# Kernel tuning notes

Hardware: AMD Instinct MI355X
Metric: run time of the kernel (lower is better)

## Reference

```python
import jax, jax.numpy as jnp
import numpy as np
import math

B, S = 4, 1024
V, D, L, H, F, MAXLEN = 32000, 1024, 6, 16, 4096, 2048
DH = D // H
NUM_BUCKETS, MAX_DIST = 32, 256
REL_SCALE = 64.0 ** 0.5
EPS = 1e-5


def setup_inputs() -> dict:
    key = jax.random.key(0)
    ks = iter(jax.random.split(key, 32))
    sd = 0.02
    inp = {
        'src': jax.random.randint(next(ks), (B, S), 0, V),
        'src_mask': jnp.ones((B, 1, 1, S), dtype=jnp.int32),
        'tok_emb': jax.random.normal(next(ks), (V, D), jnp.float32) * sd,
        'pos_emb': jax.random.normal(next(ks), (MAXLEN, D), jnp.float32) * sd,
        'Wq': jax.random.normal(next(ks), (L, D, D), jnp.float32) * sd,
        'bq': jnp.zeros((L, D), jnp.float32),
        'Wk': jax.random.normal(next(ks), (L, D, D), jnp.float32) * sd,
        'bk': jnp.zeros((L, D), jnp.float32),
        'Wv': jax.random.normal(next(ks), (L, D, D), jnp.float32) * sd,
        'bv': jnp.zeros((L, D), jnp.float32),
        'Wo': jax.random.normal(next(ks), (L, D, D), jnp.float32) * sd,
        'bo': jnp.zeros((L, D), jnp.float32),
        'rel_bias': jax.random.normal(next(ks), (L, NUM_BUCKETS, H), jnp.float32) * sd,
        'ln1_g': jnp.ones((L, D), jnp.float32),
        'ln1_b': jnp.zeros((L, D), jnp.float32),
        'W1': jax.random.normal(next(ks), (L, D, F), jnp.float32) * sd,
        'b1': jnp.zeros((L, F), jnp.float32),
        'W2': jax.random.normal(next(ks), (L, F, D), jnp.float32) * sd,
        'b2': jnp.zeros((L, D), jnp.float32),
        'ln2_g': jnp.ones((L, D), jnp.float32),
        'ln2_b': jnp.zeros((L, D), jnp.float32),
    }
    return inp


def _rel_pos_bucket(seq_len):
    # non-causal bucketing (T5-style), matching the torch source
    q = jnp.arange(seq_len)
    k = jnp.arange(seq_len)
    n = q[:, None] - k[None, :]          # == -(k - q)
    nb = NUM_BUCKETS // 2                # 16
    ret = (n < 0).astype(jnp.int32) * nb
    n = jnp.abs(n)
    max_exact = nb // 2                  # 8
    is_small = n < max_exact
    val_large = max_exact + (
        jnp.log(jnp.maximum(n, 1).astype(jnp.float32) / max_exact)
        / math.log(MAX_DIST / max_exact) * (nb - max_exact)
    ).astype(jnp.int32)
    val_large = jnp.minimum(val_large, nb - 1)
    return ret + jnp.where(is_small, n, val_large)  # [S,S] in [0,32)


def _layer_norm(x, g, b):
    mu = jnp.mean(x, axis=-1, keepdims=True)
    var = jnp.var(x, axis=-1, keepdims=True)
    return (x - mu) * jax.lax.rsqrt(var + EPS) * g + b


def reference(src, src_mask, tok_emb, pos_emb, Wq, bq, Wk, bk, Wv, bv, Wo, bo,
              rel_bias, ln1_g, ln1_b, W1, b1, W2, b2, ln2_g, ln2_b):
    seq_len = src.shape[1]
    bucket = _rel_pos_bucket(seq_len)                      # [S,S] int
    x = tok_emb[src] * jnp.sqrt(jnp.float32(D)) + pos_emb[jnp.arange(seq_len)][None]
    scale = jnp.sqrt(jnp.float32(DH))
    neg = jnp.float32(-1e10)

    def layer(x, p):
        (wq, bq_, wk, bk_, wv, bv_, wo, bo_, rb, g1, b1_, w1, bb1, w2, bb2, g2, b2_) = p
        Q = (x @ wq + bq_).reshape(B, seq_len, H, DH)
        K = (x @ wk + bk_).reshape(B, seq_len, H, DH)
        Vv = (x @ wv + bv_).reshape(B, seq_len, H, DH)
        energy = jnp.einsum('bqhd,bkhd->bhqk', Q, K) / scale
        energy = jnp.where(src_mask == 0, neg, energy)
        bias = rb[bucket]                                  # [S,S,H]
        energy = energy + jnp.transpose(bias, (2, 0, 1))[None] * REL_SCALE
        attn = jax.nn.softmax(energy, axis=-1)
        o = jnp.einsum('bhqk,bkhd->bqhd', attn, Vv).reshape(B, seq_len, D)
        o = o @ wo + bo_
        x = _layer_norm(x + o, g1, b1_)
        f = jax.nn.relu(x @ w1 + bb1) @ w2 + bb2
        x = _layer_norm(x + f, g2, b2_)
        return x, None

    params = (Wq, bq, Wk, bk, Wv, bv, Wo, bo, rel_bias,
              ln1_g, ln1_b, W1, b1, W2, b2, ln2_g, ln2_b)
    x, _ = jax.lax.scan(layer, x, params)
    return x
```

## Files before the change

### kernel.cpp

```cpp
#include <hip/hip_runtime.h>

#define B_ 4
#define S_ 1024
#define D_ 1024
#define F_ 4096
#define H_ 16
#define L_ 6
#define M_ (B_*S_)

typedef unsigned short u16;
typedef __attribute__((ext_vector_type(4))) unsigned short u16x4;
typedef __attribute__((ext_vector_type(8))) short s16x8;
typedef __attribute__((ext_vector_type(8))) __bf16 bf16x8;
typedef __attribute__((ext_vector_type(4))) float f32x4;

typedef const __attribute__((address_space(1))) unsigned int gu32;
typedef __attribute__((address_space(3))) unsigned int su32;

__device__ __forceinline__ u16 f2bf(float f) {
  union { float f; unsigned u; } v; v.f = f;
  unsigned u = v.u;
  return (u16)((u + 0x7fffu + ((u >> 16) & 1u)) >> 16);
}

__device__ __forceinline__ f32x4 mfma16(s16x8 a, s16x8 b, f32x4 c) {
  return __builtin_amdgcn_mfma_f32_16x16x32_bf16(
      __builtin_bit_cast(bf16x8, a), __builtin_bit_cast(bf16x8, b), c, 0, 0, 0);
}

__device__ __forceinline__ void gload16(const void* g, void* s) {
  __builtin_amdgcn_global_load_lds((gu32*)g, (su32*)s, 16, 0, 0);
}

__device__ __forceinline__ s16x8 lds_swz(const u16* base, int row, int cb) {
  const int addr = row * 128 + (cb ^ ((row & 7) << 4));
  return *(const s16x8*)((const char*)base + addr);
}

__global__ __launch_bounds__(256) void transpose_cvt(
    const float* __restrict__ src, u16* __restrict__ dst, int R, int Cc)
{
  __shared__ float t[32][33];
  const int c0 = blockIdx.x * 32, r0 = blockIdx.y * 32;
  const int tx = threadIdx.x & 31, ty = threadIdx.x >> 5;
#pragma unroll
  for (int i = 0; i < 4; i++)
    t[ty + 8 * i][tx] = src[(size_t)(r0 + ty + 8 * i) * Cc + c0 + tx];
  __syncthreads();
#pragma unroll
  for (int i = 0; i < 4; i++)
    dst[(size_t)(c0 + ty + 8 * i) * R + r0 + tx] = f2bf(t[tx][ty + 8 * i]);
}

__global__ __launch_bounds__(256) void transpose4(
    const float* __restrict__ Wq, const float* __restrict__ Wk,
    const float* __restrict__ Wv, const float* __restrict__ Wo,
    u16* __restrict__ WTqkv, u16* __restrict__ WTo)
{
  __shared__ float t[32][33];
  const int z = blockIdx.z;
  const float* src = (z == 0) ? Wq : (z == 1) ? Wk : (z == 2) ? Wv : Wo;
  u16* dst = (z < 3) ? WTqkv + (size_t)z * D_ * D_ : WTo;
  const int c0 = blockIdx.x * 32, r0 = blockIdx.y * 32;
  const int tx = threadIdx.x & 31, ty = threadIdx.x >> 5;
#pragma unroll
  for (int i = 0; i < 4; i++)
    t[ty + 8 * i][tx] = src[(size_t)(r0 + ty + 8 * i) * D_ + c0 + tx];
  __syncthreads();
#pragma unroll
  for (int i = 0; i < 4; i++)
    dst[(size_t)(c0 + ty + 8 * i) * D_ + r0 + tx] = f2bf(t[tx][ty + 8 * i]);
}

template<int OUTMODE>
__device__ __forceinline__ void gemm128_body(
    const u16* __restrict__ A, const u16* __restrict__ Bt,
    const float* __restrict__ bias, float* __restrict__ Cf,
    u16* __restrict__ Ch, int N, int K, int kbeg, int kend, float scale)
{
  __shared__ __align__(16) u16 As[128 * 64];
  __shared__ __align__(16) u16 Bs[128 * 64];
  const int tid = threadIdx.x, lane = tid & 63, w = tid >> 6;
  const int bm = blockIdx.x * 128, bn = blockIdx.y * 128;
  const int wm = (w >> 1) * 64, wn = (w & 1) * 64;

  f32x4 acc[4][4];
#pragma unroll
  for (int i = 0; i < 4; i++)
#pragma unroll
    for (int j = 0; j < 4; j++) acc[i][j] = {0.f, 0.f, 0.f, 0.f};

  for (int k0 = kbeg; k0 < kend; k0 += 64) {
    __syncthreads();
#pragma unroll
    for (int i = 0; i < 4; i++) {
      const int flat = i * 4096 + w * 1024 + lane * 16;
      const int row = flat >> 7, ce = (flat & 127) >> 1;
      gload16(A + (size_t)(bm + row) * K + k0 + ce, As + i * 2048 + w * 512);
      gload16(Bt + (size_t)(bn + row) * K + k0 + ce, Bs + i * 2048 + w * 512);
    }
    __syncthreads();
#pragma unroll
    for (int kk = 0; kk < 2; kk++) {
      s16x8 af[4], bf[4];
#pragma unroll
      for (int mf = 0; mf < 4; mf++)
        af[mf] = *(const s16x8*)&As[(wm + mf * 16 + (lane & 15)) * 64 + kk * 32 + (lane >> 4) * 8];
#pragma unroll
      for (int nf = 0; nf < 4; nf++)
        bf[nf] = *(const s16x8*)&Bs[(wn + nf * 16 + (lane & 15)) * 64 + kk * 32 + (lane >> 4) * 8];
#pragma unroll
      for (int mf = 0; mf < 4; mf++)
#pragma unroll
        for (int nf = 0; nf < 4; nf++)
          acc[mf][nf] = mfma16(af[mf], bf[nf], acc[mf][nf]);
    }
  }
#pragma unroll
  for (int nf = 0; nf < 4; nf++) {
    const int col = bn + wn + nf * 16 + (lane & 15);
    const float bv = (OUTMODE == 0) ? 0.f : bias[col];
#pragma unroll
    for (int mf = 0; mf < 4; mf++) {
#pragma unroll
      for (int j = 0; j < 4; j++) {
        const int row = bm + wm + mf * 16 + ((lane >> 4) << 2) + j;
        float v = acc[mf][nf][j];
        if (OUTMODE == 0) {
          Cf[(size_t)row * N + col] = v;
        } else {
          v = (v + bv) * scale;
          if (OUTMODE == 2) v = fmaxf(v, 0.f);
          Ch[(size_t)row * N + col] = f2bf(v);
        }
      }
    }
  }
}

__global__ __launch_bounds__(256, 3) void gemm_qkv(
    const u16* __restrict__ A, const u16* __restrict__ WT,
    const float* __restrict__ bq, const float* __restrict__ bk,
    const float* __restrict__ bv, u16* __restrict__ Out)
{
  const int z = blockIdx.z;
  const float* bias = (z == 0) ? bq : (z == 1) ? bk : bv;
  gemm128_body<1>(A, WT + (size_t)z * D_ * D_, bias, nullptr,
                  Out + (size_t)z * M_ * D_, D_, D_, 0, D_,
                  (z == 0) ? 0.125f : 1.0f);
}

__global__ __launch_bounds__(256, 3) void gemm_ffn1(
    const u16* __restrict__ A, const u16* __restrict__ WT,
    const float* __restrict__ bias, u16* __restrict__ Out)
{
  gemm128_body<2>(A, WT, bias, nullptr, Out, F_, D_, 0, D_, 1.0f);
}

__global__ __launch_bounds__(256, 3) void gemm_splitk(
    const u16* __restrict__ A, const u16* __restrict__ WT,
    float* __restrict__ P, int N, int K)
{
  const int z = blockIdx.z;
  const int half = K >> 1;
  gemm128_body<0>(A, WT, nullptr, P + (size_t)z * M_ * (size_t)N, nullptr,
                  N, K, z * half, z * half + half, 1.0f);
}

__global__ __launch_bounds__(256) void vt_transpose(
    const u16* __restrict__ Vb, u16* __restrict__ Vt)
{
  __shared__ u16 t[64][66];
  const int s0 = blockIdx.x * 64;
  const int bh = blockIdx.y;
  const int b = bh >> 4, h = bh & 15;
  const int tid = threadIdx.x;
  const int row = tid >> 2;
  const int c0 = (tid & 3) * 16;
  const u16* src = Vb + (size_t)(b * S_ + s0 + row) * D_ + h * 64 + c0;
  *(s16x8*)&t[row][c0] = *(const s16x8*)src;
  *(s16x8*)&t[row][c0 + 8] = *(const s16x8*)(src + 8);
  __syncthreads();
  const int dh = tid >> 2;
  const int sc = (tid & 3) * 16;
  s16x8 a, bv;
#pragma unroll
  for (int u = 0; u < 8; u++) a[u] = (short)t[sc + u][dh];
#pragma unroll
  for (int u = 0; u < 8; u++) bv[u] = (short)t[sc + 8 + u][dh];
  u16* dst = Vt + (size_t)(bh * 64 + dh) * S_ + s0 + sc;
  *(s16x8*)dst = a;
  *(s16x8*)(dst + 8) = bv;
}

__global__ __launch_bounds__(256, 4) void attn_kernel(
    const u16* __restrict__ Qb, const u16* __restrict__ Kb,
    const u16* __restrict__ Vt, const int* __restrict__ mask,
    const float* __restrict__ rb, u16* __restrict__ AO)
{
  __shared__ float lut[2048];
  __shared__ __align__(16) u16 Ks[64 * 64];
  __shared__ __align__(16) u16 Vs[64 * 64];
  __shared__ __align__(16) u16 Ps[4][16 * 68];

  const int tid = threadIdx.x;
  const int lane = tid & 63;
  const int w = tid >> 6;
  const int bh = blockIdx.x;
  const int b = bh >> 4, h = bh & 15;
  const int q0 = blockIdx.y * 64 + w * 16;
  const int bS = b * S_, hh = h * 64;

  for (int idx = tid; idx < 2048; idx += 256) {
    const int rel = idx - 1024;
    const int ret = rel < 0 ? 16 : 0;
    const int n = rel < 0 ? -rel : rel;
    int bu;
    if (n < 8) bu = ret + n;
    else {
      const float t = logf((float)n * 0.125f) * (8.0f / 3.4657359027997265f);
      int vl = 8 + (int)t;
      if (vl > 15) vl = 15;
      bu = ret + vl;
    }
    lut[idx] = rb[bu * 16 + h] * 8.0f;
  }

  s16x8 qf[2];
#pragma unroll
  for (int kk = 0; kk < 2; kk++)
    qf[kk] = *(const s16x8*)(Qb + (size_t)(bS + q0 + (lane & 15)) * D_ + hh +
                             kk * 32 + (lane >> 4) * 8);

  f32x4 oacc[4];
#pragma unroll
  for (int i = 0; i < 4; i++) oacc[i] = {0.f, 0.f, 0.f, 0.f};
  float rm[4], rl[4];
#pragma unroll
  for (int j = 0; j < 4; j++) { rm[j] = -3e38f; rl[j] = 0.f; }

  for (int kt = 0; kt < S_; kt += 64) {
    __syncthreads();
#pragma unroll
    for (int i = 0; i < 2; i++) {
      const int flat = i * 4096 + w * 1024 + lane * 16;
      const int row = flat >> 7;
      const int ce = ((flat & 127) ^ ((row & 7) << 4)) >> 1;
      gload16(Kb + (size_t)(bS + kt + row) * D_ + hh + ce, Ks + i * 2048 + w * 512);
      gload16(Vt + (size_t)(bh * 64 + row) * S_ + kt + ce, Vs + i * 2048 + w * 512);
    }
    __syncthreads();

    f32x4 sacc[4];
#pragma unroll
    for (int i = 0; i < 4; i++) sacc[i] = {0.f, 0.f, 0.f, 0.f};
#pragma unroll
    for (int kk = 0; kk < 2; kk++) {
      const int cb = kk * 64 + (lane >> 4) * 16;
#pragma unroll
      for (int nf = 0; nf < 4; nf++) {
        const s16x8 kb = lds_swz(Ks, nf * 16 + (lane & 15), cb);
        sacc[nf] = mfma16(qf[kk], kb, sacc[nf]);
      }
    }

    int km[4];
#pragma unroll
    for (int nf = 0; nf < 4; nf++)
      km[nf] = mask[bS + kt + nf * 16 + (lane & 15)];

    const int lidx0 = q0 + (lane >> 4) * 4 + 1024 - kt - (lane & 15);
#pragma unroll
    for (int j = 0; j < 4; j++) {
      const int lrow = ((lane >> 4) << 2) + j;
      float sc[4];
      float mx = -3e38f;
#pragma unroll
      for (int nf = 0; nf < 4; nf++) {
        float s = (km[nf] == 0) ? -1e10f : sacc[nf][j];
        s += lut[lidx0 + j - nf * 16];
        sc[nf] = s;
        mx = fmaxf(mx, s);
      }
      mx = fmaxf(mx, __shfl_xor(mx, 1));
      mx = fmaxf(mx, __shfl_xor(mx, 2));
      mx = fmaxf(mx, __shfl_xor(mx, 4));
      mx = fmaxf(mx, __shfl_xor(mx, 8));
      const float m_new = fmaxf(rm[j], mx);
      const float fs = __expf(rm[j] - m_new);
      rm[j] = m_new;
      float psum = 0.f;
#pragma unroll
      for (int nf = 0; nf < 4; nf++) {
        const float p = __expf(sc[nf] - m_new);
        psum += p;
        Ps[w][lrow * 68 + nf * 16 + (lane & 15)] = f2bf(p);
      }
      psum += __shfl_xor(psum, 1);
      psum += __shfl_xor(psum, 2);
      psum += __shfl_xor(psum, 4);
      psum += __shfl_xor(psum, 8);
      rl[j] = rl[j] * fs + psum;
#pragma unroll
      for (int df = 0; df < 4; df++) oacc[df][j] *= fs;
    }

#pragma unroll
    for (int kk = 0; kk < 2; kk++) {
      const s16x8 pa = *(const s16x8*)&Ps[w][(lane & 15) * 68 + kk * 32 + (lane >> 4) * 8];
      const int cb = kk * 64 + (lane >> 4) * 16;
#pragma unroll
      for (int df = 0; df < 4; df++) {
        const s16x8 vb = lds_swz(Vs, df * 16 + (lane & 15), cb);
        oacc[df] = mfma16(pa, vb, oacc[df]);
      }
    }
  }

  float inv[4];
#pragma unroll
  for (int j = 0; j < 4; j++) inv[j] = 1.0f / rl[j];
#pragma unroll
  for (int df = 0; df < 4; df++)
#pragma unroll
    for (int j = 0; j < 4; j++) {
      const int qrow = q0 + ((lane >> 4) << 2) + j;
      AO[(size_t)(bS + qrow) * D_ + hh + df * 16 + (lane & 15)] =
          f2bf(oacc[df][j] * inv[j]);
    }
}

__global__ __launch_bounds__(256) void ln_fused(
    const float* __restrict__ X, const float* __restrict__ P0,
    const float* __restrict__ P1, const float* __restrict__ bias,
    const float* __restrict__ g, const float* __restrict__ be,
    float* __restrict__ Yf, u16* __restrict__ Yh)
{
  const int row = blockIdx.x;
  const int tid = threadIdx.x;
  const float4 xv = ((const float4*)(X + (size_t)row * D_))[tid];
  const float4 p0 = ((const float4*)(P0 + (size_t)row * D_))[tid];
  const float4 p1 = ((const float4*)(P1 + (size_t)row * D_))[tid];
  const float4 bb = ((const float4*)bias)[tid];
  const float v0 = xv.x + p0.x + p1.x + bb.x;
  const float v1 = xv.y + p0.y + p1.y + bb.y;
  const float v2 = xv.z + p0.z + p1.z + bb.z;
  const float v3 = xv.w + p0.w + p1.w + bb.w;
  float sum = v0 + v1 + v2 + v3;
  float ss = v0 * v0 + v1 * v1 + v2 * v2 + v3 * v3;
#pragma unroll
  for (int o = 1; o < 64; o <<= 1) {
    sum += __shfl_xor(sum, o);
    ss += __shfl_xor(ss, o);
  }
  __shared__ float s1[4], s2[4];
  if ((tid & 63) == 0) { s1[tid >> 6] = sum; s2[tid >> 6] = ss; }
  __syncthreads();
  sum = s1[0] + s1[1] + s1[2] + s1[3];
  ss = s2[0] + s2[1] + s2[2] + s2[3];
  const float mu = sum * (1.f / D_);
  const float var = ss * (1.f / D_) - mu * mu;
  const float rstd = rsqrtf(var + 1e-5f);
  const float4 gv = ((const float4*)g)[tid];
  const float4 bv = ((const float4*)be)[tid];
  float4 y;
  y.x = (v0 - mu) * rstd * gv.x + bv.x;
  y.y = (v1 - mu) * rstd * gv.y + bv.y;
  y.z = (v2 - mu) * rstd * gv.z + bv.z;
  y.w = (v3 - mu) * rstd * gv.w + bv.w;
  ((float4*)(Yf + (size_t)row * D_))[tid] = y;
  u16x4 hv;
  hv.x = f2bf(y.x); hv.y = f2bf(y.y); hv.z = f2bf(y.z); hv.w = f2bf(y.w);
  ((u16x4*)(Yh + (size_t)row * D_))[tid] = hv;
}

__global__ __launch_bounds__(256) void embed_kernel(
    const int* __restrict__ src, const float* __restrict__ tok,
    const float* __restrict__ pos, float* __restrict__ X, u16* __restrict__ Xh)
{
  const int row = blockIdx.x;
  const int s = row & (S_ - 1);
  const int t = src[row];
  const int tid = threadIdx.x;
  const float4 tv = ((const float4*)(tok + (size_t)t * D_))[tid];
  const float4 pv = ((const float4*)(pos + (size_t)s * D_))[tid];
  float4 y;
  y.x = tv.x * 32.f + pv.x;
  y.y = tv.y * 32.f + pv.y;
  y.z = tv.z * 32.f + pv.z;
  y.w = tv.w * 32.f + pv.w;
  ((float4*)(X + (size_t)row * D_))[tid] = y;
  u16x4 hv;
  hv.x = f2bf(y.x); hv.y = f2bf(y.y); hv.z = f2bf(y.z); hv.w = f2bf(y.w);
  ((u16x4*)(Xh + (size_t)row * D_))[tid] = hv;
}

extern "C" void kernel_launch(void* const* d_in, const int* in_sizes, int n_in,
                              void* d_out, int out_size, void* d_ws, size_t ws_size,
                              hipStream_t stream)
{
  const int* src = (const int*)d_in[0];
  const int* mask = (const int*)d_in[1];
  const float* tok_emb = (const float*)d_in[2];
  const float* pos_emb = (const float*)d_in[3];
  const float* Wq = (const float*)d_in[4];
  const float* bq = (const float*)d_in[5];
  const float* Wk = (const float*)d_in[6];
  const float* bk = (const float*)d_in[7];
  const float* Wv = (const float*)d_in[8];
  const float* bv = (const float*)d_in[9];
  const float* Wo = (const float*)d_in[10];
  const float* bo = (const float*)d_in[11];
  const float* rb = (const float*)d_in[12];
  const float* g1 = (const float*)d_in[13];
  const float* b1n = (const float*)d_in[14];
  const float* W1 = (const float*)d_in[15];
  const float* b1f = (const float*)d_in[16];
  const float* W2 = (const float*)d_in[17];
  const float* b2f = (const float*)d_in[18];
  const float* g2 = (const float*)d_in[19];
  const float* b2n = (const float*)d_in[20];
  float* out = (float*)d_out;

  char* ws = (char*)d_ws;
  const size_t MB = 1ull << 20;
  float* xb   = (float*)(ws + 0);
  u16*   xb16 = (u16*)(ws + 16 * MB);
  u16*   Qb16 = (u16*)(ws + 24 * MB);
  u16*   Kb16 = (u16*)(ws + 32 * MB);
  u16*   Vb16 = (u16*)(ws + 40 * MB);
  u16*   Vt16 = (u16*)(ws + 48 * MB);
  u16*   AO16 = (u16*)(ws + 40 * MB);
  float* OPp  = (float*)(ws + 48 * MB);
  u16*   Hb16 = (u16*)(ws + 24 * MB);
  float* Fp   = (float*)(ws + 56 * MB);
  u16* WTqkv  = (u16*)(ws + 88 * MB);
  u16* WTo    = (u16*)(ws + 94 * MB);
  u16* WT1    = (u16*)(ws + 96 * MB);
  u16* WT2    = (u16*)(ws + 104 * MB);

  embed_kernel<<<M_, 256, 0, stream>>>(src, tok_emb, pos_emb, xb, xb16);

  for (int l = 0; l < L_; l++) {
    const size_t oDD = (size_t)l * D_ * D_;
    const size_t oDF = (size_t)l * D_ * F_;

    transpose4<<<dim3(32, 32, 4), 256, 0, stream>>>(
        Wq + oDD, Wk + oDD, Wv + oDD, Wo + oDD, WTqkv, WTo);
    transpose_cvt<<<dim3(F_ / 32, D_ / 32), 256, 0, stream>>>(W1 + oDF, WT1, D_, F_);
    transpose_cvt<<<dim3(D_ / 32, F_ / 32), 256, 0, stream>>>(W2 + oDF, WT2, F_, D_);

    gemm_qkv<<<dim3(M_ / 128, D_ / 128, 3), 256, 0, stream>>>(
        xb16, WTqkv, bq + l * D_, bk + l * D_, bv + l * D_, Qb16);

    vt_transpose<<<dim3(S_ / 64, B_ * H_), 256, 0, stream>>>(Vb16, Vt16);

    attn_kernel<<<dim3(B_ * H_, S_ / 64), 256, 0, stream>>>(
        Qb16, Kb16, Vt16, mask, rb + l * 32 * H_, AO16);

    gemm_splitk<<<dim3(M_ / 128, D_ / 128, 2), 256, 0, stream>>>(
        AO16, WTo, OPp, D_, D_);

    ln_fused<<<M_, 256, 0, stream>>>(
        xb, OPp, OPp + (size_t)M_ * D_, bo + l * D_,
        g1 + l * D_, b1n + l * D_, xb, xb16);

    gemm_ffn1<<<dim3(M_ / 128, F_ / 128), 256, 0, stream>>>(
        xb16, WT1, b1f + l * F_, Hb16);

    gemm_splitk<<<dim3(M_ / 128, D_ / 128, 2), 256, 0, stream>>>(
        Hb16, WT2, Fp, D_, F_);

    ln_fused<<<M_, 256, 0, stream>>>(
        xb, Fp, Fp + (size_t)M_ * D_, b2f + l * D_,
        g2 + l * D_, b2n + l * D_, (l == L_ - 1) ? out : xb, xb16);
  }
}
```

Before: 1.511 ms.

## Replace 128x128 GEMM with double-buffered 256x256 pipelined MFMA kernel and split-K 4

```diff
diff --git a/kernel.cpp b/kernel.cpp
--- a/kernel.cpp
+++ b/kernel.cpp
@@ -32,99 +32,133 @@
   __builtin_amdgcn_global_load_lds((gu32*)g, (su32*)s, 16, 0, 0);
 }
 
-__device__ __forceinline__ s16x8 lds_swz(const u16* base, int row, int cb) {
-  const int addr = row * 128 + (cb ^ ((row & 7) << 4));
-  return *(const s16x8*)((const char*)base + addr);
-}
-
-__global__ __launch_bounds__(256) void transpose_cvt(
-    const float* __restrict__ src, u16* __restrict__ dst, int R, int Cc)
-{
-  __shared__ float t[32][33];
-  const int c0 = blockIdx.x * 32, r0 = blockIdx.y * 32;
-  const int tx = threadIdx.x & 31, ty = threadIdx.x >> 5;
-#pragma unroll
-  for (int i = 0; i < 4; i++)
-    t[ty + 8 * i][tx] = src[(size_t)(r0 + ty + 8 * i) * Cc + c0 + tx];
-  __syncthreads();
-#pragma unroll
-  for (int i = 0; i < 4; i++)
-    dst[(size_t)(c0 + ty + 8 * i) * R + r0 + tx] = f2bf(t[tx][ty + 8 * i]);
-}
-
-__global__ __launch_bounds__(256) void transpose4(
-    const float* __restrict__ Wq, const float* __restrict__ Wk,
-    const float* __restrict__ Wv, const float* __restrict__ Wo,
-    u16* __restrict__ WTqkv, u16* __restrict__ WTo)
-{
-  __shared__ float t[32][33];
-  const int z = blockIdx.z;
-  const float* src = (z == 0) ? Wq : (z == 1) ? Wk : (z == 2) ? Wv : Wo;
-  u16* dst = (z < 3) ? WTqkv + (size_t)z * D_ * D_ : WTo;
-  const int c0 = blockIdx.x * 32, r0 = blockIdx.y * 32;
-  const int tx = threadIdx.x & 31, ty = threadIdx.x >> 5;
-#pragma unroll
-  for (int i = 0; i < 4; i++)
-    t[ty + 8 * i][tx] = src[(size_t)(r0 + ty + 8 * i) * D_ + c0 + tx];
-  __syncthreads();
-#pragma unroll
-  for (int i = 0; i < 4; i++)
-    dst[(size_t)(c0 + ty + 8 * i) * D_ + r0 + tx] = f2bf(t[tx][ty + 8 * i]);
-}
+__device__ __forceinline__ s16x8 readfrag(const u16* half, int r, int kk, int hi4) {
+  const int c = (kk * 64 + hi4 * 16) ^ ((r & 7) << 4);
+  return *(const s16x8*)((const char*)half + r * 128 + c);
+}
+
+__device__ __forceinline__ void stage_half(
+    const u16* __restrict__ src, int ldk, u16* lds_half, int w, int lane)
+{
+#pragma unroll
+  for (int j = 0; j < 2; j++) {
+    const int flat = j * 8192 + w * 1024 + lane * 16;
+    const int row = flat >> 7;
+    const int kb = (flat & 127) ^ ((row & 7) << 4);
+    gload16(src + (size_t)row * ldk + (kb >> 1), lds_half + j * 4096 + w * 512);
+  }
+}
+
+#define BAR     asm volatile("s_barrier" ::: "memory")
+#define PH_PRE  asm volatile("s_barrier" ::: "memory"); __builtin_amdgcn_s_setprio(1)
+#define PH_POST __builtin_amdgcn_s_setprio(0); __builtin_amdgcn_sched_barrier(0)
+#define VM4     asm volatile("s_waitcnt vmcnt(4)" ::: "memory")
+#define VM0     asm volatile("s_waitcnt vmcnt(0)" ::: "memory")
+
+#define READ_B(bufhalf) do { \
+  _Pragma("unroll") for (int nf = 0; nf < 4; nf++) \
+  _Pragma("unroll") for (int kk = 0; kk < 2; kk++) \
+    bfr[nf][kk] = readfrag(bufhalf, rb0 + nf * 16 + lo16, kk, hi4); } while (0)
+#define READ_A(bufhalf, Q) do { \
+  _Pragma("unroll") for (int m = 0; m < 2; m++) \
+  _Pragma("unroll") for (int kk = 0; kk < 2; kk++) \
+    af[m][kk] = readfrag(bufhalf, (2 * (Q) + m) * 16 + lo16, kk, hi4); } while (0)
+#define DO_MFMA(Q) do { \
+  _Pragma("unroll") for (int kk = 0; kk < 2; kk++) \
+  _Pragma("unroll") for (int m = 0; m < 2; m++) \
+  _Pragma("unroll") for (int nf = 0; nf < 4; nf++) \
+    acc[2 * (Q) + m][nf] = mfma16(af[m][kk], bfr[nf][kk], acc[2 * (Q) + m][nf]); } while (0)
 
 template<int OUTMODE>
-__device__ __forceinline__ void gemm128_body(
+__device__ __forceinline__ void gemm256_body(
     const u16* __restrict__ A, const u16* __restrict__ Bt,
     const float* __restrict__ bias, float* __restrict__ Cf,
-    u16* __restrict__ Ch, int N, int K, int kbeg, int kend, float scale)
-{
-  __shared__ __align__(16) u16 As[128 * 64];
-  __shared__ __align__(16) u16 Bs[128 * 64];
+    u16* __restrict__ Ch, int N, int K, int kbeg, int kslice, float scale)
+{
+  __shared__ __align__(16) u16 As[2][2][8192];
+  __shared__ __align__(16) u16 Bs[2][2][8192];
   const int tid = threadIdx.x, lane = tid & 63, w = tid >> 6;
-  const int bm = blockIdx.x * 128, bn = blockIdx.y * 128;
-  const int wm = (w >> 1) * 64, wn = (w & 1) * 64;
-
-  f32x4 acc[4][4];
-#pragma unroll
-  for (int i = 0; i < 4; i++)
+  const int wr = w >> 2, wc = w & 3;
+  const int lo16 = lane & 15, hi4 = lane >> 4;
+  const int bm = blockIdx.x * 256, bn = blockIdx.y * 256;
+  const int rb0 = (wc & 1) * 64;
+
+  const u16* Abase = A + (size_t)bm * K + kbeg;
+  const u16* Bbase = Bt + (size_t)bn * K + kbeg;
+  const size_t h1 = (size_t)128 * K;
+  const int NT = kslice >> 6, NI = NT >> 1;
+
+  f32x4 acc[8][4];
+#pragma unroll
+  for (int i = 0; i < 8; i++)
 #pragma unroll
     for (int j = 0; j < 4; j++) acc[i][j] = {0.f, 0.f, 0.f, 0.f};
 
-  for (int k0 = kbeg; k0 < kend; k0 += 64) {
-    __syncthreads();
-#pragma unroll
-    for (int i = 0; i < 4; i++) {
-      const int flat = i * 4096 + w * 1024 + lane * 16;
-      const int row = flat >> 7, ce = (flat & 127) >> 1;
-      gload16(A + (size_t)(bm + row) * K + k0 + ce, As + i * 2048 + w * 512);
-      gload16(Bt + (size_t)(bn + row) * K + k0 + ce, Bs + i * 2048 + w * 512);
-    }
-    __syncthreads();
-#pragma unroll
-    for (int kk = 0; kk < 2; kk++) {
-      s16x8 af[4], bf[4];
-#pragma unroll
-      for (int mf = 0; mf < 4; mf++)
-        af[mf] = *(const s16x8*)&As[(wm + mf * 16 + (lane & 15)) * 64 + kk * 32 + (lane >> 4) * 8];
-#pragma unroll
-      for (int nf = 0; nf < 4; nf++)
-        bf[nf] = *(const s16x8*)&Bs[(wn + nf * 16 + (lane & 15)) * 64 + kk * 32 + (lane >> 4) * 8];
-#pragma unroll
-      for (int mf = 0; mf < 4; mf++)
-#pragma unroll
-        for (int nf = 0; nf < 4; nf++)
-          acc[mf][nf] = mfma16(af[mf], bf[nf], acc[mf][nf]);
-    }
-  }
+  stage_half(Abase,           K, As[0][0], w, lane);
+  stage_half(Abase + h1,      K, As[0][1], w, lane);
+  stage_half(Bbase,           K, Bs[0][0], w, lane);
+  stage_half(Bbase + h1,      K, Bs[0][1], w, lane);
+  stage_half(Abase + 64,      K, As[1][0], w, lane);
+  stage_half(Abase + h1 + 64, K, As[1][1], w, lane);
+  stage_half(Bbase + 64,      K, Bs[1][0], w, lane);
+  stage_half(Bbase + h1 + 64, K, Bs[1][1], w, lane);
+  asm volatile("s_waitcnt vmcnt(8)" ::: "memory");
+  BAR;
+
+  const u16* Ae = As[0][wr]; const u16* Ao = As[1][wr];
+  const u16* Be = Bs[0][wc >> 1]; const u16* Bo = Bs[1][wc >> 1];
+  s16x8 af[2][2], bfr[4][2];
+
+  for (int it = 0; it < NI - 1; ++it) {
+    READ_B(Be); READ_A(Ae, 0);
+    if (it > 0) {
+      stage_half(Abase +      (size_t)(2 * it + 1) * 64, K, As[1][0], w, lane);
+      stage_half(Abase + h1 + (size_t)(2 * it + 1) * 64, K, As[1][1], w, lane);
+    }
+    PH_PRE; DO_MFMA(0); PH_POST; BAR;
+    READ_A(Ae, 1);
+    stage_half(Bbase +      (size_t)(2 * it + 2) * 64, K, Bs[0][0], w, lane);
+    PH_PRE; DO_MFMA(1); PH_POST; BAR;
+    READ_A(Ae, 2);
+    stage_half(Bbase + h1 + (size_t)(2 * it + 2) * 64, K, Bs[0][1], w, lane);
+    PH_PRE; DO_MFMA(2); PH_POST; BAR;
+    READ_A(Ae, 3);
+    PH_PRE; DO_MFMA(3); PH_POST; VM4; BAR;
+    READ_B(Bo); READ_A(Ao, 0);
+    stage_half(Abase +      (size_t)(2 * it + 2) * 64, K, As[0][0], w, lane);
+    stage_half(Abase + h1 + (size_t)(2 * it + 2) * 64, K, As[0][1], w, lane);
+    PH_PRE; DO_MFMA(0); PH_POST; BAR;
+    READ_A(Ao, 1);
+    stage_half(Bbase +      (size_t)(2 * it + 3) * 64, K, Bs[1][0], w, lane);
+    PH_PRE; DO_MFMA(1); PH_POST; BAR;
+    READ_A(Ao, 2);
+    stage_half(Bbase + h1 + (size_t)(2 * it + 3) * 64, K, Bs[1][1], w, lane);
+    PH_PRE; DO_MFMA(2); PH_POST; BAR;
+    READ_A(Ao, 3);
+    PH_PRE; DO_MFMA(3); PH_POST; VM4; BAR;
+  }
+  READ_B(Be); READ_A(Ae, 0);
+  stage_half(Abase +      (size_t)(NT - 1) * 64, K, As[1][0], w, lane);
+  stage_half(Abase + h1 + (size_t)(NT - 1) * 64, K, As[1][1], w, lane);
+  PH_PRE; DO_MFMA(0); PH_POST; BAR;
+  READ_A(Ae, 1);             PH_PRE; DO_MFMA(1); PH_POST; BAR;
+  READ_A(Ae, 2);             PH_PRE; DO_MFMA(2); PH_POST; BAR;
+  READ_A(Ae, 3);             PH_PRE; DO_MFMA(3); PH_POST; VM0; BAR;
+  READ_B(Bo); READ_A(Ao, 0); PH_PRE; DO_MFMA(0); PH_POST; BAR;
+  READ_A(Ao, 1);             PH_PRE; DO_MFMA(1); PH_POST; BAR;
+  READ_A(Ao, 2);             PH_PRE; DO_MFMA(2); PH_POST; BAR;
+  READ_A(Ao, 3);             PH_PRE; DO_MFMA(3); PH_POST;
+
+  const int row0 = bm + wr * 128, col0 = bn + wc * 64;
 #pragma unroll
   for (int nf = 0; nf < 4; nf++) {
-    const int col = bn + wn + nf * 16 + (lane & 15);
+    const int col = col0 + nf * 16 + lo16;
     const float bv = (OUTMODE == 0) ? 0.f : bias[col];
 #pragma unroll
-    for (int mf = 0; mf < 4; mf++) {
+    for (int mf = 0; mf < 8; mf++) {
 #pragma unroll
       for (int j = 0; j < 4; j++) {
-        const int row = bm + wm + mf * 16 + ((lane >> 4) << 2) + j;
+        const int row = row0 + mf * 16 + hi4 * 4 + j;
         float v = acc[mf][nf][j];
         if (OUTMODE == 0) {
           Cf[(size_t)row * N + col] = v;
@@ -138,33 +172,68 @@
   }
 }
 
-__global__ __launch_bounds__(256, 3) void gemm_qkv(
+__global__ __launch_bounds__(512, 2) void gemm_qkv(
     const u16* __restrict__ A, const u16* __restrict__ WT,
     const float* __restrict__ bq, const float* __restrict__ bk,
     const float* __restrict__ bv, u16* __restrict__ Out)
 {
   const int z = blockIdx.z;
   const float* bias = (z == 0) ? bq : (z == 1) ? bk : bv;
-  gemm128_body<1>(A, WT + (size_t)z * D_ * D_, bias, nullptr,
+  gemm256_body<1>(A, WT + (size_t)z * D_ * D_, bias, nullptr,
                   Out + (size_t)z * M_ * D_, D_, D_, 0, D_,
                   (z == 0) ? 0.125f : 1.0f);
 }
 
-__global__ __launch_bounds__(256, 3) void gemm_ffn1(
+__global__ __launch_bounds__(512, 2) void gemm_ffn1(
     const u16* __restrict__ A, const u16* __restrict__ WT,
     const float* __restrict__ bias, u16* __restrict__ Out)
 {
-  gemm128_body<2>(A, WT, bias, nullptr, Out, F_, D_, 0, D_, 1.0f);
-}
-
-__global__ __launch_bounds__(256, 3) void gemm_splitk(
+  gemm256_body<2>(A, WT, bias, nullptr, Out, F_, D_, 0, D_, 1.0f);
+}
+
+__global__ __launch_bounds__(512, 2) void gemm_splitk4(
     const u16* __restrict__ A, const u16* __restrict__ WT,
     float* __restrict__ P, int N, int K)
 {
   const int z = blockIdx.z;
-  const int half = K >> 1;
-  gemm128_body<0>(A, WT, nullptr, P + (size_t)z * M_ * (size_t)N, nullptr,
-                  N, K, z * half, z * half + half, 1.0f);
+  const int q = K >> 2;
+  gemm256_body<0>(A, WT, nullptr, P + (size_t)z * M_ * (size_t)N, nullptr,
+                  N, K, z * q, q, 1.0f);
+}
+
+__global__ __launch_bounds__(256) void transpose_cvt(
+    const float* __restrict__ src, u16* __restrict__ dst, int R, int Cc)
+{
+  __shared__ float t[32][33];
+  const int c0 = blockIdx.x * 32, r0 = blockIdx.y * 32;
+  const int tx = threadIdx.x & 31, ty = threadIdx.x >> 5;
+#pragma unroll
+  for (int i = 0; i < 4; i++)
+    t[ty + 8 * i][tx] = src[(size_t)(r0 + ty + 8 * i) * Cc + c0 + tx];
+  __syncthreads();
+#pragma unroll
+  for (int i = 0; i < 4; i++)
+    dst[(size_t)(c0 + ty + 8 * i) * R + r0 + tx] = f2bf(t[tx][ty + 8 * i]);
+}
+
+__global__ __launch_bounds__(256) void transpose4(
+    const float* __restrict__ Wq, const float* __restrict__ Wk,
+    const float* __restrict__ Wv, const float* __restrict__ Wo,
+    u16* __restrict__ WTqkv, u16* __restrict__ WTo)
+{
+  __shared__ float t[32][33];
+  const int z = blockIdx.z;
+  const float* src = (z == 0) ? Wq : (z == 1) ? Wk : (z == 2) ? Wv : Wo;
+  u16* dst = (z < 3) ? WTqkv + (size_t)z * D_ * D_ : WTo;
+  const int c0 = blockIdx.x * 32, r0 = blockIdx.y * 32;
+  const int tx = threadIdx.x & 31, ty = threadIdx.x >> 5;
+#pragma unroll
+  for (int i = 0; i < 4; i++)
+    t[ty + 8 * i][tx] = src[(size_t)(r0 + ty + 8 * i) * D_ + c0 + tx];
+  __syncthreads();
+#pragma unroll
+  for (int i = 0; i < 4; i++)
+    dst[(size_t)(c0 + ty + 8 * i) * D_ + r0 + tx] = f2bf(t[tx][ty + 8 * i]);
 }
 
 __global__ __launch_bounds__(256) void vt_transpose(
@@ -193,6 +262,11 @@
   *(s16x8*)(dst + 8) = bv;
 }
 
+__device__ __forceinline__ s16x8 lds_swz(const u16* base, int row, int cb) {
+  const int addr = row * 128 + (cb ^ ((row & 7) << 4));
+  return *(const s16x8*)((const char*)base + addr);
+}
+
 __global__ __launch_bounds__(256, 4) void attn_kernel(
     const u16* __restrict__ Qb, const u16* __restrict__ Kb,
     const u16* __restrict__ Vt, const int* __restrict__ mask,
@@ -330,22 +404,25 @@
     }
 }
 
-__global__ __launch_bounds__(256) void ln_fused(
-    const float* __restrict__ X, const float* __restrict__ P0,
-    const float* __restrict__ P1, const float* __restrict__ bias,
-    const float* __restrict__ g, const float* __restrict__ be,
-    float* __restrict__ Yf, u16* __restrict__ Yh)
+__global__ __launch_bounds__(256) void ln_fused4(
+    const float* __restrict__ X, const float* __restrict__ P,
+    const float* __restrict__ bias, const float* __restrict__ g,
+    const float* __restrict__ be, float* __restrict__ Yf, u16* __restrict__ Yh)
 {
   const int row = blockIdx.x;
   const int tid = threadIdx.x;
-  const float4 xv = ((const float4*)(X + (size_t)row * D_))[tid];
-  const float4 p0 = ((const float4*)(P0 + (size_t)row * D_))[tid];
-  const float4 p1 = ((const float4*)(P1 + (size_t)row * D_))[tid];
+  const size_t off = (size_t)row * D_;
+  const size_t pstride = (size_t)M_ * D_;
+  const float4 xv = ((const float4*)(X + off))[tid];
+  const float4 p0 = ((const float4*)(P + off))[tid];
+  const float4 p1 = ((const float4*)(P + pstride + off))[tid];
+  const float4 p2 = ((const float4*)(P + 2 * pstride + off))[tid];
+  const float4 p3 = ((const float4*)(P + 3 * pstride + off))[tid];
   const float4 bb = ((const float4*)bias)[tid];
-  const float v0 = xv.x + p0.x + p1.x + bb.x;
-  const float v1 = xv.y + p0.y + p1.y + bb.y;
-  const float v2 = xv.z + p0.z + p1.z + bb.z;
-  const float v3 = xv.w + p0.w + p1.w + bb.w;
+  const float v0 = xv.x + p0.x + p1.x + p2.x + p3.x + bb.x;
+  const float v1 = xv.y + p0.y + p1.y + p2.y + p3.y + bb.y;
+  const float v2 = xv.z + p0.z + p1.z + p2.z + p3.z + bb.z;
+  const float v3 = xv.w + p0.w + p1.w + p2.w + p3.w + bb.w;
   float sum = v0 + v1 + v2 + v3;
   float ss = v0 * v0 + v1 * v1 + v2 * v2 + v3 * v3;
 #pragma unroll
@@ -368,10 +445,10 @@
   y.y = (v1 - mu) * rstd * gv.y + bv.y;
   y.z = (v2 - mu) * rstd * gv.z + bv.z;
   y.w = (v3 - mu) * rstd * gv.w + bv.w;
-  ((float4*)(Yf + (size_t)row * D_))[tid] = y;
+  ((float4*)(Yf + off))[tid] = y;
   u16x4 hv;
   hv.x = f2bf(y.x); hv.y = f2bf(y.y); hv.z = f2bf(y.z); hv.w = f2bf(y.w);
-  ((u16x4*)(Yh + (size_t)row * D_))[tid] = hv;
+  ((u16x4*)(Yh + off))[tid] = hv;
 }
 
 __global__ __launch_bounds__(256) void embed_kernel(
@@ -430,14 +507,13 @@
   u16*   Kb16 = (u16*)(ws + 32 * MB);
   u16*   Vb16 = (u16*)(ws + 40 * MB);
   u16*   Vt16 = (u16*)(ws + 48 * MB);
-  u16*   AO16 = (u16*)(ws + 40 * MB);
-  float* OPp  = (float*)(ws + 48 * MB);
+  u16*   AO16 = (u16*)(ws + 56 * MB);
+  float* Pp   = (float*)(ws + 64 * MB);
+  u16*   WTqkv= (u16*)(ws + 128 * MB);
+  u16*   WTo  = (u16*)(ws + 134 * MB);
+  u16*   WT1  = (u16*)(ws + 136 * MB);
+  u16*   WT2  = (u16*)(ws + 144 * MB);
   u16*   Hb16 = (u16*)(ws + 24 * MB);
-  float* Fp   = (float*)(ws + 56 * MB);
-  u16* WTqkv  = (u16*)(ws + 88 * MB);
-  u16* WTo    = (u16*)(ws + 94 * MB);
-  u16* WT1    = (u16*)(ws + 96 * MB);
-  u16* WT2    = (u16*)(ws + 104 * MB);
 
   embed_kernel<<<M_, 256, 0, stream>>>(src, tok_emb, pos_emb, xb, xb16);
 
@@ -450,7 +526,7 @@
     transpose_cvt<<<dim3(F_ / 32, D_ / 32), 256, 0, stream>>>(W1 + oDF, WT1, D_, F_);
     transpose_cvt<<<dim3(D_ / 32, F_ / 32), 256, 0, stream>>>(W2 + oDF, WT2, F_, D_);
 
-    gemm_qkv<<<dim3(M_ / 128, D_ / 128, 3), 256, 0, stream>>>(
+    gemm_qkv<<<dim3(M_ / 256, D_ / 256, 3), 512, 0, stream>>>(
         xb16, WTqkv, bq + l * D_, bk + l * D_, bv + l * D_, Qb16);
 
     vt_transpose<<<dim3(S_ / 64, B_ * H_), 256, 0, stream>>>(Vb16, Vt16);
@@ -458,21 +534,20 @@
     attn_kernel<<<dim3(B_ * H_, S_ / 64), 256, 0, stream>>>(
         Qb16, Kb16, Vt16, mask, rb + l * 32 * H_, AO16);
 
-    gemm_splitk<<<dim3(M_ / 128, D_ / 128, 2), 256, 0, stream>>>(
-        AO16, WTo, OPp, D_, D_);
-
-    ln_fused<<<M_, 256, 0, stream>>>(
-        xb, OPp, OPp + (size_t)M_ * D_, bo + l * D_,
-        g1 + l * D_, b1n + l * D_, xb, xb16);
-
-    gemm_ffn1<<<dim3(M_ / 128, F_ / 128), 256, 0, stream>>>(
+    gemm_splitk4<<<dim3(M_ / 256, D_ / 256, 4), 512, 0, stream>>>(
+        AO16, WTo, Pp, D_, D_);
+
+    ln_fused4<<<M_, 256, 0, stream>>>(
+        xb, Pp, bo + l * D_, g1 + l * D_, b1n + l * D_, xb, xb16);
+
+    gemm_ffn1<<<dim3(M_ / 256, F_ / 256), 512, 0, stream>>>(
         xb16, WT1, b1f + l * F_, Hb16);
 
-    gemm_splitk<<<dim3(M_ / 128, D_ / 128, 2), 256, 0, stream>>>(
-        Hb16, WT2, Fp, D_, F_);
-
-    ln_fused<<<M_, 256, 0, stream>>>(
-        xb, Fp, Fp + (size_t)M_ * D_, b2f + l * D_,
-        g2 + l * D_, b2n + l * D_, (l == L_ - 1) ? out : xb, xb16);
-  }
-}
+    gemm_splitk4<<<dim3(M_ / 256, D_ / 256, 4), 512, 0, stream>>>(
+        Hb16, WT2, Pp, D_, F_);
+
+    ln_fused4<<<M_, 256, 0, stream>>>(
+        xb, Pp, b2f + l * D_, g2 + l * D_, b2n + l * D_,
+        (l == L_ - 1) ? out : xb, xb16);
+  }
+}
```

Result: slower. 1.623 ms (+7.4%).
